# Optimization experiments

Hardware: AMD Instinct MI355X
Metric: run time of the kernel (lower is better)

The kernel has to match this reference:

```python
import jax, jax.numpy as jnp
import numpy as np

NUM_HEADS = 32
EMB = 4096
HEAD_DIM = EMB // NUM_HEADS  # 128
BATCH = 2
SEQ = 2048


def setup_inputs() -> dict:
    key = jax.random.key(0)
    k1, k2, k3 = jax.random.split(key, 3)
    x = jax.random.normal(k1, (BATCH, SEQ, EMB), dtype=jnp.float32)
    # Linear weights stored as [in, out] (equivalent to torch [out,in].T)
    w_atten = jax.random.normal(k2, (EMB, 3 * EMB), dtype=jnp.float32) * (EMB ** -0.5)
    w_proj = jax.random.normal(k3, (EMB, EMB), dtype=jnp.float32) * (EMB ** -0.5)
    # Standard LLaMA rotary frequencies: theta_i = 10000^{-2i/d}
    half = HEAD_DIM // 2
    inv_freq = 1.0 / (10000.0 ** (np.arange(0, half, dtype=np.float32) * 2.0 / HEAD_DIM))
    t = np.arange(SEQ, dtype=np.float32)
    angles = np.outer(t, inv_freq)  # [SEQ, half]
    freqs_cos = jnp.asarray(np.cos(angles), dtype=jnp.float32)
    freqs_sin = jnp.asarray(np.sin(angles), dtype=jnp.float32)
    return {"x": x, "w_atten": w_atten, "w_proj": w_proj,
            "freqs_cos": freqs_cos, "freqs_sin": freqs_sin}


def _apply_rope(t, cos, sin):
    # t: [B, S, H, D]; cos/sin: [S, D/2] -> complex rotation on (even, odd) pairs
    B, S, H, D = t.shape
    tr = t.reshape(B, S, H, D // 2, 2)
    tr_r, tr_i = tr[..., 0], tr[..., 1]
    c = cos[None, :, None, :]
    s = sin[None, :, None, :]
    out_r = tr_r * c - tr_i * s
    out_i = tr_r * s + tr_i * c
    return jnp.stack([out_r, out_i], axis=-1).reshape(B, S, H, D)


def reference(x, w_atten, w_proj, freqs_cos, freqs_sin):
    B, S, D = x.shape
    H, Hd = NUM_HEADS, HEAD_DIM
    qkv = x @ w_atten                       # [B, S, 3D]
    q, k, v = jnp.split(qkv, 3, axis=-1)
    q = q.reshape(B, S, H, Hd)
    k = k.reshape(B, S, H, Hd)              # n_kv_heads == num_heads, n_rep == 1
    v = v.reshape(B, S, H, Hd)
    q = _apply_rope(q, freqs_cos, freqs_sin)
    k = _apply_rope(k, freqs_cos, freqs_sin)
    att = jnp.einsum('bqhd,bkhd->bhqk', q, k) * (1.0 / jnp.sqrt(jnp.float32(Hd)))
    causal = jnp.tril(jnp.ones((S, S), dtype=bool))
    att = jnp.where(causal[None, None], att, jnp.float32(-jnp.inf))
    att = jax.nn.softmax(att, axis=-1)
    y = jnp.einsum('bhqk,bkhd->bqhd', att, v).reshape(B, S, D)
    return y @ w_proj
```

## Files before the change

### kernel.cpp

```cpp
#include <hip/hip_runtime.h>

typedef __bf16 bfrag8 __attribute__((ext_vector_type(8)));
typedef float f32x4 __attribute__((ext_vector_type(4)));
typedef unsigned int u32x4 __attribute__((ext_vector_type(4)));
typedef unsigned short ush;

__device__ __forceinline__ float bf2f(ush s) {
    union { unsigned int u; float f; } un; un.u = ((unsigned int)s) << 16; return un.f;
}
__device__ __forceinline__ ush f2bf(float f) {
    union { float f; unsigned int u; } un; un.f = f;
    unsigned int u = un.u;
    u += 0x7fffu + ((u >> 16) & 1u);
    return (ush)(u >> 16);
}

typedef __attribute__((address_space(3))) unsigned int lds_uint;
typedef __attribute__((address_space(1))) const unsigned int glob_uint;

__device__ __forceinline__ void async_copy16(const ush* g, ush* l) {
    __builtin_amdgcn_global_load_lds((glob_uint*)g, (lds_uint*)l, 16, 0, 0);
}

__global__ __launch_bounds__(256)
void conv_bf(const float* __restrict__ X, ush* __restrict__ Xb, long n8)
{
    long i = (long)blockIdx.x * 256 + threadIdx.x;
    if (i >= n8) return;
    const float4 a = *reinterpret_cast<const float4*>(&X[i * 8]);
    const float4 b = *reinterpret_cast<const float4*>(&X[i * 8 + 4]);
    u32x4 r;
    r[0] = (unsigned int)f2bf(a.x) | ((unsigned int)f2bf(a.y) << 16);
    r[1] = (unsigned int)f2bf(a.z) | ((unsigned int)f2bf(a.w) << 16);
    r[2] = (unsigned int)f2bf(b.x) | ((unsigned int)f2bf(b.y) << 16);
    r[3] = (unsigned int)f2bf(b.z) | ((unsigned int)f2bf(b.w) << 16);
    *reinterpret_cast<u32x4*>(&Xb[i * 8]) = r;
}

__global__ __launch_bounds__(256)
void transpose_bf(const float* __restrict__ W, ush* __restrict__ Wt, int K, int N)
{
    __shared__ __align__(16) ush T[64][72];
    const int tid = threadIdx.x;
    const long kb = (long)blockIdx.y * 64;
    const long nb = (long)blockIdx.x * 64;

    const int r  = tid >> 4;
    const int c4 = tid & 15;
    #pragma unroll
    for (int i = 0; i < 4; ++i) {
        int row = r + i * 16;
        float4 v = *reinterpret_cast<const float4*>(&W[(kb + row) * (long)N + nb + c4 * 4]);
        T[c4 * 4 + 0][row] = f2bf(v.x);
        T[c4 * 4 + 1][row] = f2bf(v.y);
        T[c4 * 4 + 2][row] = f2bf(v.z);
        T[c4 * 4 + 3][row] = f2bf(v.w);
    }
    __syncthreads();

    const int n  = tid >> 3;
    const int kc = tid & 7;
    #pragma unroll
    for (int i = 0; i < 2; ++i) {
        int row = n + i * 32;
        *reinterpret_cast<u32x4*>(&Wt[(nb + row) * (long)K + kb + kc * 8]) =
            *reinterpret_cast<const u32x4*>(&T[row][kc * 8]);
    }
}

__global__ __launch_bounds__(256)
void vtrans_kernel(const ush* __restrict__ qkv, ush* __restrict__ vt)
{
    __shared__ __align__(16) ush T[128 * 64];
    const int tid = threadIdx.x;
    const int s0 = blockIdx.x * 64;
    const int bh = blockIdx.y;
    const int b = bh >> 5, h = bh & 31;
    const ush* vbase = qkv + (long)b * 2048 * 12288 + 8192 + h * 128;

    #pragma unroll
    for (int i = 0; i < 4; ++i) {
        int c = tid + i * 256;
        int sl = c & 63, cd = c >> 6;
        u32x4 v = *reinterpret_cast<const u32x4*>(&vbase[(long)(s0 + sl) * 12288 + cd * 8]);
        const ush* pv = reinterpret_cast<const ush*>(&v);
        #pragma unroll
        for (int j = 0; j < 8; ++j)
            T[(cd * 8 + j) * 64 + sl] = pv[j];
    }
    __syncthreads();

    #pragma unroll
    for (int i = 0; i < 4; ++i) {
        int c = tid + i * 256;
        int d = c >> 3, sc = c & 7;
        *reinterpret_cast<u32x4*>(&vt[((long)bh * 128 + d) * 2048 + s0 + sc * 8]) =
            *reinterpret_cast<const u32x4*>(&T[d * 64 + sc * 8]);
    }
}

#define GBM 256
#define GBN 256
#define GBK 64

__device__ __forceinline__ void store_out(float* p, float v) { *p = v; }
__device__ __forceinline__ void store_out(ush* p, float v)   { *p = f2bf(v); }

__device__ __forceinline__ bfrag8 lds_frag(const ush* Sb, int row, int c16, int sx) {
    return *reinterpret_cast<const bfrag8*>(&Sb[row * 64 + (((c16) ^ sx) << 3)]);
}

__device__ __forceinline__ void stage_half(const ush* __restrict__ G, long row0, long ld,
                                           long kcol, ush* lds_tile, int half,
                                           int wave, int lane)
{
    #pragma unroll
    for (int inst = 0; inst < 2; ++inst) {
        const int base_row = half * 128 + wave * 16 + inst * 8;
        const int r = base_row + (lane >> 3);
        const int c = ((lane & 7) ^ ((lane >> 3) & 7)) << 3;
        async_copy16(&G[(row0 + r) * ld + kcol + c], &lds_tile[base_row * 64]);
    }
}

#define LOAD_AF(QM) { _Pragma("unroll") for (int mi = 0; mi < 4; ++mi) \
    _Pragma("unroll") for (int ks = 0; ks < 2; ++ks) \
        af[mi][ks] = lds_frag(SA, wm * 128 + (QM) * 64 + mi * 16 + lrow, ks * 4 + quad, sx); }

#define LOAD_BF(QN) { _Pragma("unroll") for (int ni = 0; ni < 2; ++ni) \
    _Pragma("unroll") for (int ks = 0; ks < 2; ++ks) \
        bf[ni][ks] = lds_frag(SB, wn * 64 + (QN) * 32 + ni * 16 + lrow, ks * 4 + quad, sx); }

#define MFMA_QUAD(QM, QN) { \
    __builtin_amdgcn_s_setprio(1); \
    _Pragma("unroll") for (int mi = 0; mi < 4; ++mi) \
    _Pragma("unroll") for (int ni = 0; ni < 2; ++ni) \
    _Pragma("unroll") for (int ks = 0; ks < 2; ++ks) \
        acc[(QM) * 4 + mi][(QN) * 2 + ni] = __builtin_amdgcn_mfma_f32_16x16x32_bf16( \
            af[mi][ks], bf[ni][ks], acc[(QM) * 4 + mi][(QN) * 2 + ni], 0, 0, 0); \
    __builtin_amdgcn_s_setprio(0); }

template <typename OUT>
__global__ __launch_bounds__(512, 2)
void gemm_bt8(const ush* __restrict__ A, const ush* __restrict__ B,
              OUT* __restrict__ C, int M, int N, int K)
{
    __shared__ __align__(16) ush S[65536];

    const int tid  = threadIdx.x;
    const int wave = tid >> 6, lane = tid & 63;
    const int wm = wave >> 2, wn = wave & 3;
    const int lrow = lane & 15, quad = lane >> 4;
    const int sx = lrow & 7;

    const int gx = gridDim.x;
    const int nwg = gx * gridDim.y;
    int lid = blockIdx.y * gx + blockIdx.x;
    lid = (lid & 7) * (nwg >> 3) + (lid >> 3);
    const long m0 = (long)(lid / gx) * GBM;
    const long n0 = (long)(lid % gx) * GBN;
    const long lK = K;
    const int NT = K / GBK;

    f32x4 acc[8][4];
    const f32x4 fzero = {0.f, 0.f, 0.f, 0.f};
    #pragma unroll
    for (int i = 0; i < 8; ++i)
        #pragma unroll
        for (int j = 0; j < 4; ++j) acc[i][j] = fzero;

    bfrag8 af[4][2], bf[2][2];

    stage_half(A, m0, lK, 0, S,         0, wave, lane);
    stage_half(A, m0, lK, 0, S,         1, wave, lane);
    stage_half(B, n0, lK, 0, S + 16384, 0, wave, lane);
    stage_half(B, n0, lK, 0, S + 16384, 1, wave, lane);
    stage_half(A, m0, lK, GBK, S + 32768, 0, wave, lane);
    asm volatile("s_waitcnt vmcnt(2)" ::: "memory");
    __builtin_amdgcn_s_barrier();

    for (int t = 0; t < NT; ++t) {
        const int p = t & 1;
        ush* SA  = S + p * 32768;
        ush* SB  = SA + 16384;
        ush* SAn = S + (p ^ 1) * 32768;
        ush* SBn = SAn + 16384;
        const long kc1 = (long)(t + 1) * GBK;
        const long kc2 = (long)(t + 2) * GBK;
        const bool st1 = (t + 1) < NT;
        const bool st2 = (t + 2) < NT;

        LOAD_AF(0); LOAD_BF(0);
        if (st1) stage_half(A, m0, lK, kc1, SAn, 1, wave, lane);
        __builtin_amdgcn_s_barrier();
        MFMA_QUAD(0, 0);
        __builtin_amdgcn_s_barrier();

        LOAD_BF(1);
        if (st1) stage_half(B, n0, lK, kc1, SBn, 0, wave, lane);
        __builtin_amdgcn_s_barrier();
        MFMA_QUAD(0, 1);
        __builtin_amdgcn_s_barrier();

        LOAD_AF(1);
        if (st1) stage_half(B, n0, lK, kc1, SBn, 1, wave, lane);
        __builtin_amdgcn_s_barrier();
        MFMA_QUAD(1, 1);
        __builtin_amdgcn_s_barrier();

        LOAD_BF(0);
        if (st2) stage_half(A, m0, lK, kc2, SA, 0, wave, lane);
        __builtin_amdgcn_s_barrier();
        MFMA_QUAD(1, 0);
        __builtin_amdgcn_s_barrier();

        if (st1) {
            if (st2) asm volatile("s_waitcnt vmcnt(2)" ::: "memory");
            else     asm volatile("s_waitcnt vmcnt(0)" ::: "memory");
            __builtin_amdgcn_s_barrier();
        }
    }

    #pragma unroll
    for (int mi = 0; mi < 8; ++mi)
        #pragma unroll
        for (int ni = 0; ni < 4; ++ni)
            #pragma unroll
            for (int r = 0; r < 4; ++r) {
                long row = m0 + wm * 128 + mi * 16 + quad * 4 + r;
                long col = n0 + wn * 64 + ni * 16 + lrow;
                store_out(&C[row * (long)N + col], acc[mi][ni][r]);
            }
}

__global__ void rope_kernel(ush* __restrict__ qkv,
                            const float* __restrict__ cosb, const float* __restrict__ sinb)
{
    int idx = blockIdx.x * 256 + threadIdx.x;
    int i = idx & 63;
    int h = (idx >> 6) & 31;
    int s = (idx >> 11) & 2047;
    int b = idx >> 22;
    float c  = cosb[s * 64 + i];
    float sn = sinb[s * 64 + i];
    long base = ((long)(b * 2048 + s)) * 12288 + h * 128 + 2 * i;
    float qr = bf2f(qkv[base]), qi = bf2f(qkv[base + 1]);
    qkv[base]     = f2bf(qr * c - qi * sn);
    qkv[base + 1] = f2bf(qr * sn + qi * c);
    float kr = bf2f(qkv[base + 4096]), ki = bf2f(qkv[base + 4097]);
    qkv[base + 4096] = f2bf(kr * c - ki * sn);
    qkv[base + 4097] = f2bf(kr * sn + ki * c);
}

#define LDK 136
#define LDV 72
#define LDP 72

__global__ __launch_bounds__(256)
void attn_kernel(const ush* __restrict__ qkv, const ush* __restrict__ vt,
                 ush* __restrict__ y)
{
    __shared__ ush Ks[64 * LDK];
    __shared__ ush Vt[128 * LDV];
    __shared__ ush Ps[128 * LDP];

    const int bh = blockIdx.x;
    const int qt = 15 - blockIdx.y;
    const int b = bh >> 5, h = bh & 31;
    const int tid = threadIdx.x, wave = tid >> 6, lane = tid & 63;
    const int lrow = lane & 15, quad = lane >> 4;
    const int q0 = qt * 128;
    const long rs = 12288;
    const ush* qb = qkv + (long)b * 2048 * rs + h * 128;
    const ush* kb = qb + 4096;
    const ush* vtb = vt + (long)bh * 128 * 2048;
    const float scale = 0.08838834764831845f;

    bfrag8 qf[2][4];
    #pragma unroll
    for (int mi = 0; mi < 2; ++mi)
        #pragma unroll
        for (int kk = 0; kk < 4; ++kk) {
            long qrow = q0 + wave * 32 + mi * 16 + lrow;
            qf[mi][kk] = *reinterpret_cast<const bfrag8*>(&qb[qrow * rs + kk * 32 + quad * 8]);
        }

    const f32x4 fzero = {0.f, 0.f, 0.f, 0.f};
    f32x4 O[2][8];
    #pragma unroll
    for (int mi = 0; mi < 2; ++mi)
        #pragma unroll
        for (int dt = 0; dt < 8; ++dt) O[mi][dt] = fzero;
    f32x4 mst[2], lst[2];
    #pragma unroll
    for (int mi = 0; mi < 2; ++mi)
        #pragma unroll
        for (int r = 0; r < 4; ++r) { mst[mi][r] = -1e30f; lst[mi][r] = 0.f; }

    const int ntiles = 2 * qt + 2;
    for (int nt = 0; nt < ntiles; ++nt) {
        const int kv0 = nt * 64;
        #pragma unroll
        for (int i = 0; i < 4; ++i) {
            int c = tid + i * 256;
            int row = c >> 4, cc = c & 15;
            u32x4 v = *reinterpret_cast<const u32x4*>(&kb[(long)(kv0 + row) * rs + cc * 8]);
            *reinterpret_cast<u32x4*>(&Ks[row * LDK + cc * 8]) = v;
        }
        #pragma unroll
        for (int i = 0; i < 4; ++i) {
            int c = tid + i * 256;
            int row = c >> 3, cc = c & 7;
            u32x4 v = *reinterpret_cast<const u32x4*>(&vtb[(long)row * 2048 + kv0 + cc * 8]);
            *reinterpret_cast<u32x4*>(&Vt[row * LDV + cc * 8]) = v;
        }
        __syncthreads();

        f32x4 sv[2][4];
        #pragma unroll
        for (int ni = 0; ni < 4; ++ni) {
            bfrag8 kf[4];
            #pragma unroll
            for (int kk = 0; kk < 4; ++kk)
                kf[kk] = *reinterpret_cast<const bfrag8*>(&Ks[(ni * 16 + lrow) * LDK + kk * 32 + quad * 8]);
            #pragma unroll
            for (int mi = 0; mi < 2; ++mi) {
                f32x4 a = fzero;
                #pragma unroll
                for (int kk = 0; kk < 4; ++kk)
                    a = __builtin_amdgcn_mfma_f32_16x16x32_bf16(qf[mi][kk], kf[kk], a, 0, 0, 0);
                sv[mi][ni] = a;
            }
        }

        #pragma unroll
        for (int mi = 0; mi < 2; ++mi)
            #pragma unroll
            for (int ni = 0; ni < 4; ++ni)
                #pragma unroll
                for (int r = 0; r < 4; ++r) {
                    int q  = q0 + wave * 32 + mi * 16 + quad * 4 + r;
                    int kv = kv0 + ni * 16 + lrow;
                    float x = sv[mi][ni][r] * scale;
                    sv[mi][ni][r] = (kv <= q) ? x : -1e30f;
                }

        #pragma unroll
        for (int mi = 0; mi < 2; ++mi) {
            f32x4 rmax;
            #pragma unroll
            for (int r = 0; r < 4; ++r)
                rmax[r] = fmaxf(fmaxf(sv[mi][0][r], sv[mi][1][r]),
                                fmaxf(sv[mi][2][r], sv[mi][3][r]));
            #pragma unroll
            for (int off = 1; off < 16; off <<= 1)
                #pragma unroll
                for (int r = 0; r < 4; ++r)
                    rmax[r] = fmaxf(rmax[r], __shfl_xor(rmax[r], off, 64));

            f32x4 mnew, alpha;
            #pragma unroll
            for (int r = 0; r < 4; ++r) {
                mnew[r]  = fmaxf(mst[mi][r], rmax[r]);
                alpha[r] = __expf(mst[mi][r] - mnew[r]);
            }
            f32x4 rsum = fzero;
            #pragma unroll
            for (int ni = 0; ni < 4; ++ni)
                #pragma unroll
                for (int r = 0; r < 4; ++r) {
                    float p = __expf(sv[mi][ni][r] - mnew[r]);
                    sv[mi][ni][r] = p;
                    rsum[r] += p;
                }
            #pragma unroll
            for (int off = 1; off < 16; off <<= 1)
                #pragma unroll
                for (int r = 0; r < 4; ++r)
                    rsum[r] += __shfl_xor(rsum[r], off, 64);
            #pragma unroll
            for (int r = 0; r < 4; ++r) {
                lst[mi][r] = lst[mi][r] * alpha[r] + rsum[r];
                mst[mi][r] = mnew[r];
            }
            #pragma unroll
            for (int dt = 0; dt < 8; ++dt)
                #pragma unroll
                for (int r = 0; r < 4; ++r)
                    O[mi][dt][r] *= alpha[r];
            #pragma unroll
            for (int ni = 0; ni < 4; ++ni)
                #pragma unroll
                for (int r = 0; r < 4; ++r)
                    Ps[(wave * 32 + mi * 16 + quad * 4 + r) * LDP + ni * 16 + lrow]
                        = f2bf(sv[mi][ni][r]);
        }


        bfrag8 pf[2][2];
        #pragma unroll
        for (int mi = 0; mi < 2; ++mi)
            #pragma unroll
            for (int nk = 0; nk < 2; ++nk)
                pf[mi][nk] = *reinterpret_cast<const bfrag8*>(
                    &Ps[(wave * 32 + mi * 16 + lrow) * LDP + nk * 32 + quad * 8]);
        #pragma unroll
        for (int dt = 0; dt < 8; ++dt) {
            bfrag8 vf[2];
            #pragma unroll
            for (int nk = 0; nk < 2; ++nk)
                vf[nk] = *reinterpret_cast<const bfrag8*>(
                    &Vt[(dt * 16 + lrow) * LDV + nk * 32 + quad * 8]);
            #pragma unroll
            for (int mi = 0; mi < 2; ++mi)
                #pragma unroll
                for (int nk = 0; nk < 2; ++nk)
                    O[mi][dt] = __builtin_amdgcn_mfma_f32_16x16x32_bf16(pf[mi][nk], vf[nk], O[mi][dt], 0, 0, 0);
        }
        __syncthreads();
    }

    #pragma unroll
    for (int mi = 0; mi < 2; ++mi)
        #pragma unroll
        for (int r = 0; r < 4; ++r) {
            float inv = 1.0f / lst[mi][r];
            long q = q0 + wave * 32 + mi * 16 + quad * 4 + r;
            long base = (long)(b * 2048 + q) * 4096 + h * 128 + lrow;
            #pragma unroll
            for (int dt = 0; dt < 8; ++dt)
                y[base + dt * 16] = f2bf(O[mi][dt][r] * inv);
        }
}

extern "C" void kernel_launch(void* const* d_in, const int* in_sizes, int n_in,
                              void* d_out, int out_size, void* d_ws, size_t ws_size,
                              hipStream_t stream)
{
    const float* x  = (const float*)d_in[0];
    const float* wa = (const float*)d_in[1];
    const float* wp = (const float*)d_in[2];
    const float* fc = (const float*)d_in[3];
    const float* fs = (const float*)d_in[4];
    float* out = (float*)d_out;

    char* ws = (char*)d_ws;
    ush* qkv = (ush*)ws;
    ush* xb  = (ush*)(ws + 100663296);
    ush* wat = (ush*)(ws + 134217728);
    ush* wpt = xb;
    ush* y   = wat;
    ush* vt  = (ush*)(ws + 167772160);

    conv_bf<<<8192, 256, 0, stream>>>(x, xb, 2097152);
    transpose_bf<<<dim3(12288 / 64, 4096 / 64), 256, 0, stream>>>(wa, wat, 4096, 12288);
    gemm_bt8<ush><<<dim3(12288 / GBN, 4096 / GBM), 512, 0, stream>>>(xb, wat, qkv, 4096, 12288, 4096);
    transpose_bf<<<dim3(4096 / 64, 4096 / 64), 256, 0, stream>>>(wp, wpt, 4096, 4096);
    rope_kernel<<<8388608 / 256, 256, 0, stream>>>(qkv, fc, fs);
    vtrans_kernel<<<dim3(32, 64), 256, 0, stream>>>(qkv, vt);
    attn_kernel<<<dim3(64, 16), 256, 0, stream>>>(qkv, vt, y);
    gemm_bt8<float><<<dim3(4096 / GBN, 4096 / GBM), 512, 0, stream>>>(y, wpt, out, 4096, 4096, 4096);
}
```

Measured before the change: 1.107 ms.

## Remap GEMM workgroups into per-XCD patches and restructure prefetch staging

```diff
diff --git a/kernel.cpp b/kernel.cpp
--- a/kernel.cpp
+++ b/kernel.cpp
@@ -143,7 +143,7 @@
 template <typename OUT>
 __global__ __launch_bounds__(512, 2)
 void gemm_bt8(const ush* __restrict__ A, const ush* __restrict__ B,
-              OUT* __restrict__ C, int M, int N, int K)
+              OUT* __restrict__ C, int M, int N, int K, int PH, int PW)
 {
     __shared__ __align__(16) ush S[65536];
 
@@ -154,11 +154,12 @@
     const int sx = lrow & 7;
 
     const int gx = gridDim.x;
-    const int nwg = gx * gridDim.y;
-    int lid = blockIdx.y * gx + blockIdx.x;
-    lid = (lid & 7) * (nwg >> 3) + (lid >> 3);
-    const long m0 = (long)(lid / gx) * GBM;
-    const long n0 = (long)(lid % gx) * GBN;
+    const int orig = blockIdx.y * gx + blockIdx.x;
+    const int xcd = orig & 7;
+    const int q = orig >> 3;
+    const int pcols = gx / PW;
+    const long m0 = (long)((xcd / pcols) * PH + q / PW) * GBM;
+    const long n0 = (long)((xcd % pcols) * PW + q % PW) * GBN;
     const long lK = K;
     const int NT = K / GBK;
 
@@ -171,12 +172,13 @@
 
     bfrag8 af[4][2], bf[2][2];
 
-    stage_half(A, m0, lK, 0, S,         0, wave, lane);
-    stage_half(A, m0, lK, 0, S,         1, wave, lane);
-    stage_half(B, n0, lK, 0, S + 16384, 0, wave, lane);
-    stage_half(B, n0, lK, 0, S + 16384, 1, wave, lane);
+    stage_half(A, m0, lK, 0,   S,         0, wave, lane);
+    stage_half(A, m0, lK, 0,   S,         1, wave, lane);
+    stage_half(B, n0, lK, 0,   S + 16384, 0, wave, lane);
+    stage_half(B, n0, lK, 0,   S + 16384, 1, wave, lane);
     stage_half(A, m0, lK, GBK, S + 32768, 0, wave, lane);
-    asm volatile("s_waitcnt vmcnt(2)" ::: "memory");
+    stage_half(A, m0, lK, GBK, S + 32768, 1, wave, lane);
+    asm volatile("s_waitcnt vmcnt(4)" ::: "memory");
     __builtin_amdgcn_s_barrier();
 
     for (int t = 0; t < NT; ++t) {
@@ -191,31 +193,35 @@
         const bool st2 = (t + 2) < NT;
 
         LOAD_AF(0); LOAD_BF(0);
-        if (st1) stage_half(A, m0, lK, kc1, SAn, 1, wave, lane);
+        if (st1) {
+            stage_half(B, n0, lK, kc1, SBn, 0, wave, lane);
+            stage_half(B, n0, lK, kc1, SBn, 1, wave, lane);
+        }
         __builtin_amdgcn_s_barrier();
         MFMA_QUAD(0, 0);
         __builtin_amdgcn_s_barrier();
 
         LOAD_BF(1);
-        if (st1) stage_half(B, n0, lK, kc1, SBn, 0, wave, lane);
         __builtin_amdgcn_s_barrier();
         MFMA_QUAD(0, 1);
         __builtin_amdgcn_s_barrier();
 
         LOAD_AF(1);
-        if (st1) stage_half(B, n0, lK, kc1, SBn, 1, wave, lane);
         __builtin_amdgcn_s_barrier();
         MFMA_QUAD(1, 1);
         __builtin_amdgcn_s_barrier();
 
         LOAD_BF(0);
-        if (st2) stage_half(A, m0, lK, kc2, SA, 0, wave, lane);
+        if (st2) {
+            stage_half(A, m0, lK, kc2, SA, 0, wave, lane);
+            stage_half(A, m0, lK, kc2, SA, 1, wave, lane);
+        }
         __builtin_amdgcn_s_barrier();
         MFMA_QUAD(1, 0);
         __builtin_amdgcn_s_barrier();
 
         if (st1) {
-            if (st2) asm volatile("s_waitcnt vmcnt(2)" ::: "memory");
+            if (st2) asm volatile("s_waitcnt vmcnt(4)" ::: "memory");
             else     asm volatile("s_waitcnt vmcnt(0)" ::: "memory");
             __builtin_amdgcn_s_barrier();
         }
@@ -454,10 +460,10 @@
 
     conv_bf<<<8192, 256, 0, stream>>>(x, xb, 2097152);
     transpose_bf<<<dim3(12288 / 64, 4096 / 64), 256, 0, stream>>>(wa, wat, 4096, 12288);
-    gemm_bt8<ush><<<dim3(12288 / GBN, 4096 / GBM), 512, 0, stream>>>(xb, wat, qkv, 4096, 12288, 4096);
+    gemm_bt8<ush><<<dim3(12288 / GBN, 4096 / GBM), 512, 0, stream>>>(xb, wat, qkv, 4096, 12288, 4096, 8, 12);
     transpose_bf<<<dim3(4096 / 64, 4096 / 64), 256, 0, stream>>>(wp, wpt, 4096, 4096);
     rope_kernel<<<8388608 / 256, 256, 0, stream>>>(qkv, fc, fs);
     vtrans_kernel<<<dim3(32, 64), 256, 0, stream>>>(qkv, vt);
     attn_kernel<<<dim3(64, 16), 256, 0, stream>>>(qkv, vt, y);
-    gemm_bt8<float><<<dim3(4096 / GBN, 4096 / GBM), 512, 0, stream>>>(y, wpt, out, 4096, 4096, 4096);
-}
+    gemm_bt8<float><<<dim3(4096 / GBN, 4096 / GBM), 512, 0, stream>>>(y, wpt, out, 4096, 4096, 4096, 4, 8);
+}
```

New measurement: 1.106 ms. No clear change (-0.1%).
